# Optimization experiments

Hardware: AMD Instinct MI355X
Metric: run time of the kernel (lower is better)

Reference implementation:

```python
import jax, jax.numpy as jnp
import numpy as np

B = 8       # complexes in batch
C = 32      # CDR residues per antibody
G = 2048    # antigen nodes per complex
D = 128     # encoded_dims
N_AB = B * C
N_AG = B * G
N = N_AB + N_AG
SLOPE = 0.2
EPS_BN = 1e-5


def _build_edges():
    # block-sparse bipartite edges (cdr_b x ag_b), symmetrized, + self loops
    srcs, dsts = [], []
    for b in range(B):
        ab = np.arange(b * C, (b + 1) * C)
        ag = np.arange(N_AB + b * G, N_AB + (b + 1) * G)
        g1, g2 = np.meshgrid(ab, ag, indexing='ij')
        srcs.append(g1.ravel()); dsts.append(g2.ravel())
    s = np.concatenate(srcs); d = np.concatenate(dsts)
    loops = np.arange(N)
    src = np.concatenate([s, d, loops]).astype(np.int32)
    dst = np.concatenate([d, s, loops]).astype(np.int32)
    return src, dst


def setup_inputs() -> dict:
    key = jax.random.key(0)
    ks = jax.random.split(key, 16)
    sc = 1.0 / np.sqrt(D)
    edge_src, edge_dst = _build_edges()
    return {
        'selected_ab': jax.random.normal(ks[0], (N_AB, D), jnp.float32),
        'x_ag': jax.random.normal(ks[1], (N_AG, D), jnp.float32),
        'W1': jax.random.normal(ks[2], (D, D), jnp.float32) * sc,
        'a_src1': jax.random.normal(ks[3], (D,), jnp.float32) * sc,
        'a_dst1': jax.random.normal(ks[4], (D,), jnp.float32) * sc,
        'b1': jnp.zeros((D,), jnp.float32),
        'W2': jax.random.normal(ks[5], (D, D), jnp.float32) * sc,
        'a_src2': jax.random.normal(ks[6], (D,), jnp.float32) * sc,
        'a_dst2': jax.random.normal(ks[7], (D,), jnp.float32) * sc,
        'b2': jnp.zeros((D,), jnp.float32),
        'bn_ab_g': jnp.ones((2 * D,), jnp.float32),
        'bn_ab_b': jnp.zeros((2 * D,), jnp.float32),
        'bn_ag_g': jnp.ones((2 * D,), jnp.float32),
        'bn_ag_b': jnp.zeros((2 * D,), jnp.float32),
        'fc_w': jax.random.normal(ks[8], (2 * D, 1), jnp.float32) * sc,
        'fc_b': jnp.zeros((1,), jnp.float32),
        'agfc_w': jax.random.normal(ks[9], (2 * D, 1), jnp.float32) * sc,
        'agfc_b': jnp.zeros((1,), jnp.float32),
        'edge_src': jnp.asarray(edge_src),
        'edge_dst': jnp.asarray(edge_dst),
    }


def _gat(x, W, a_s, a_d, b, src, dst):
    # PyG GATConv, heads=1, eval mode (dropout off)
    h = x @ W                                  # [N, D]
    al_s = h @ a_s                             # [N]
    al_d = h @ a_d                             # [N]
    e = jax.nn.leaky_relu(al_s[src] + al_d[dst], SLOPE)   # [E]
    m = jax.ops.segment_max(e, dst, num_segments=N)
    e = jnp.exp(e - m[dst])
    z = jax.ops.segment_sum(e, dst, num_segments=N)
    alpha = e / (z[dst] + 1e-16)
    out = jax.ops.segment_sum(h[src] * alpha[:, None], dst, num_segments=N)
    return out + b


def _bn(x, g, b):
    # training-mode batch stats (biased variance), like torch BatchNorm1d
    m = x.mean(0)
    v = ((x - m) ** 2).mean(0)
    return (x - m) / jnp.sqrt(v + EPS_BN) * g + b


def reference(selected_ab, x_ag, W1, a_src1, a_dst1, b1, W2, a_src2, a_dst2, b2,
              bn_ab_g, bn_ab_b, bn_ag_g, bn_ag_b, fc_w, fc_b, agfc_w, agfc_b,
              edge_src, edge_dst):
    x = jnp.concatenate([selected_ab, x_ag], axis=0)          # [N, D]
    x = jax.nn.relu(_gat(x, W1, a_src1, a_dst1, b1, edge_src, edge_dst))
    x = _gat(x, W2, a_src2, a_dst2, b2, edge_src, edge_dst)
    x_ab = jnp.concatenate([x[:N_AB], selected_ab], axis=1)   # [N_ab, 2D]
    x_ab = jax.nn.relu(_bn(x_ab, bn_ab_g, bn_ab_b))
    x_ab = (x_ab @ fc_w + fc_b).ravel()
    x_ag_o = jnp.concatenate([x[N_AB:], x_ag], axis=1)        # [N_ag, 2D]
    x_ag_o = jax.nn.relu(_bn(x_ag_o, bn_ag_g, bn_ag_b))
    x_ag_o = (x_ag_o @ agfc_w + agfc_b).ravel()
    return (x_ab, x_ag_o)
```

## Files before the change

kernel.cpp:

```cpp
#include <hip/hip_runtime.h>


#define N_AB 256
#define N_AG 16384
#define N_ALL 16640
#define G_AG 2048
#define SLOPE 0.2f
#define MSHIFT 20.0f
#define GRID_F 512

typedef __attribute__((ext_vector_type(4))) float f32x4;
typedef __attribute__((ext_vector_type(8))) __bf16 bf16x8;
typedef __attribute__((ext_vector_type(8))) unsigned short u16x8;
typedef unsigned short ushort_t;

__device__ __forceinline__ float bf2f(ushort_t u) {
  union { unsigned int i; float f; } v; v.i = ((unsigned int)u) << 16; return v.f;
}
__device__ __forceinline__ ushort_t f2bf(float f) {
  union { float fv; unsigned int i; } v; v.fv = f;
  unsigned int x = v.i;
  return (ushort_t)((x + 0x7fffu + ((x >> 16) & 1u)) >> 16);
}
__device__ __forceinline__ float lrelu(float x) { return x >= 0.f ? x : SLOPE * x; }
__device__ __forceinline__ float expw(float e) {
  return __expf(fminf(e, 60.f) - MSHIFT);
}
__device__ __forceinline__ float ldf(const void* p, size_t i, int f) {
  return f ? ((const float*)p)[i] : bf2f(((const ushort_t*)p)[i]);
}
__device__ __forceinline__ void ld8f(const void* p, size_t i, int f, float* o) {
  if (f) {
    const f32x4* q = (const f32x4*)((const float*)p + i);
    f32x4 a = q[0], b = q[1];
#pragma unroll
    for (int j = 0; j < 4; ++j) { o[j] = a[j]; o[j + 4] = b[j]; }
  } else {
    u16x8 v = *(const u16x8*)((const ushort_t*)p + i);
#pragma unroll
    for (int j = 0; j < 8; ++j) o[j] = bf2f(v[j]);
  }
}

__device__ __forceinline__ void gbar(unsigned* __restrict__ ctr, int t) {
  __syncthreads();
  if (t == 0) {
    __threadfence();
    atomicAdd(ctr, 1u);
    while (atomicAdd(ctr, 0u) < (unsigned)GRID_F) __builtin_amdgcn_s_sleep(2);
  }
  __syncthreads();
  __threadfence();
}

__global__ __launch_bounds__(64) void k_init(unsigned* __restrict__ ctr) {
  if (threadIdx.x < 16) ctr[threadIdx.x] = 0u;
}

#define ABP_STRIDE 72
#define AG_STRIDE 40
#define HS_OFF 5120
#define HS_STRIDE 136

__global__ __launch_bounds__(256, 2) void k_fused(
    const void* __restrict__ sel_ab, const void* __restrict__ x_ag,
    const void* __restrict__ W1, const void* __restrict__ as1,
    const void* __restrict__ ad1, const void* __restrict__ b1,
    const void* __restrict__ W2, const void* __restrict__ as2,
    const void* __restrict__ ad2, const void* __restrict__ b2,
    const void* __restrict__ gab, const void* __restrict__ bab,
    const void* __restrict__ gag, const void* __restrict__ bag,
    const void* __restrict__ fcw, const void* __restrict__ fcb,
    const void* __restrict__ agfcw, const void* __restrict__ agfcb,
    ushort_t* __restrict__ h, ushort_t* __restrict__ xb,
    ushort_t* __restrict__ W1t, ushort_t* __restrict__ W2t,
    float* __restrict__ va, float* __restrict__ als, float* __restrict__ ald,
    float* __restrict__ bnsumAG, float* __restrict__ statsAG,
    float* __restrict__ xabf, float* __restrict__ accf,
    float* __restrict__ accz,
    float* __restrict__ selpart, float* __restrict__ selpartq,
    float* __restrict__ abpart, float* __restrict__ abpartq,
    float* __restrict__ agpart, float* __restrict__ agpartq,
    unsigned* __restrict__ ctrs, void* __restrict__ out) {
  __shared__ ushort_t hT[13824];
  __shared__ float alsS[64];
  __shared__ float colsum[128], colsq[128];
  __shared__ float preLs[2][128], preLq[2][128];
  __shared__ float zsh[32], wsh[32];
  __shared__ float stA[256], stB[256], stW[256];

  int t = threadIdx.x, lane = t & 63, wid = t >> 6;
  int bx = blockIdx.x;
  int mm = lane & 15, q = lane >> 4;

  const ushort_t* selu = (const ushort_t*)sel_ab;
  int cnt = 0;
#pragma unroll
  for (int i = 0; i < 8; ++i) {
    unsigned e = (selu[lane * 8 + i] >> 7) & 0xFF;
    if (e > 0xC8) cnt++;
  }
  int f = (__popcll(__ballot(cnt > 0)) >= 3) ? 1 : 0;

  if (bx < 16) {
    const void* W = (bx < 8) ? W1 : W2;
    ushort_t* Wt = (bx < 8) ? W1t : W2t;
    int base = (bx & 7) * 2048 + t * 8;
    float o[8];
    ld8f(W, base, f, o);
#pragma unroll
    for (int j = 0; j < 8; ++j) {
      int idx = base + j;
      Wt[(idx & 127) * 128 + (idx >> 7)] = f2bf(o[j]);
    }
  } else if (bx < 32) {
    int j = bx - 16;
    const void* W   = (j < 8) ? W1 : W2;
    const void* asv = (j < 8) ? as1 : as2;
    const void* adv = (j < 8) ? ad1 : ad2;
    int vbase = (j < 8) ? 0 : 256;
    int basek = (j & 7) * 16 + wid * 4;
    float a_s0 = ldf(asv, lane, f), a_s1 = ldf(asv, lane + 64, f);
    float a_d0 = ldf(adv, lane, f), a_d1 = ldf(adv, lane + 64, f);
#pragma unroll
    for (int i = 0; i < 4; ++i) {
      int k = basek + i;
      float w0 = ldf(W, (size_t)k * 128 + lane, f);
      float w1 = ldf(W, (size_t)k * 128 + lane + 64, f);
      float ps = w0 * a_s0 + w1 * a_s1;
      float pd = w0 * a_d0 + w1 * a_d1;
#pragma unroll
      for (int o = 1; o < 64; o <<= 1) {
        ps += __shfl_xor(ps, o);
        pd += __shfl_xor(pd, o);
      }
      if (lane == 0) { va[vbase + k] = ps; va[vbase + 128 + k] = pd; }
    }
  } else if (bx < 40) {
    int j = bx - 32;
    f32x4* az = (f32x4*)(accf + (size_t)j * 4096);
    f32x4 z4 = (f32x4){0.f, 0.f, 0.f, 0.f};
    for (int i = t; i < 1024; i += 256) az[i] = z4;
    if (j == 0) { bnsumAG[t] = 0.f; bnsumAG[t + 256] = 0.f; accz[t] = 0.f; }
  } else if (bx < 48) {
    int j = bx - 40;
    int col = t & 127, rh = t >> 7;
    int r0 = j * 32 + rh * 16;
    float s = 0.f, sq = 0.f;
    for (int r = 0; r < 16; ++r) {
      float v = ldf(sel_ab, (size_t)(r0 + r) * 128 + col, f);
      s += v; sq += v * v;
    }
    preLs[rh][col] = s; preLq[rh][col] = sq;
    __syncthreads();
    if (t < 128) {
      selpart[j * 128 + t] = preLs[0][t] + preLs[1][t];
      selpartq[j * 128 + t] = preLq[0][t] + preLq[1][t];
    }
  } else if (bx < 112) {
    int j = bx - 48;
    int col = t & 127, half = t >> 7;
    int r0 = j * 256 + half * 128;
    float s = 0.f, sq = 0.f;
    for (int r = 0; r < 128; ++r) {
      float v = ldf(x_ag, (size_t)(r0 + r) * 128 + col, f);
      s += v; sq += v * v;
    }
    preLs[half][col] = s; preLq[half][col] = sq;
    __syncthreads();
    if (t < 128) {
      agpart[j * 128 + t] = preLs[0][t] + preLs[1][t];
      agpartq[j * 128 + t] = preLq[0][t] + preLq[1][t];
    }
  }
  gbar(&ctrs[0], t);

  auto gemm_tile = [&](int tile, const void* xa, int fxA, const void* xbv,
                       int fxB, const ushort_t* Wt, const float* vav) {
    int rw0 = tile * 32 + (wid >> 1) * 16;
    int ch = wid & 1;
    const void* xsrc; int roff, fx;
    if (rw0 < N_AB) { xsrc = xa; roff = rw0; fx = fxA; }
    else            { xsrc = xbv; roff = rw0 - N_AB; fx = fxB; }
    f32x4 acc[4];
#pragma unroll
    for (int b = 0; b < 4; ++b) acc[b] = (f32x4){0.f, 0.f, 0.f, 0.f};
    float pals = 0.f, pald = 0.f;
#pragma unroll
    for (int s = 0; s < 4; ++s) {
      int koff = s * 32 + q * 8;
      union { u16x8 u; bf16x8 b; } af;
      float o[8];
      ld8f(xsrc, (size_t)(roff + mm) * 128 + koff, fx, o);
#pragma unroll
      for (int j = 0; j < 8; ++j) {
        af.u[j] = f2bf(o[j]);
        pals += o[j] * vav[koff + j];
        pald += o[j] * vav[128 + koff + j];
      }
#pragma unroll
      for (int nt = 0; nt < 4; ++nt) {
        int colb = ch * 64 + nt * 16;
        bf16x8 bfr = *(const bf16x8*)(Wt + (size_t)(colb + mm) * 128 + koff);
        acc[nt] = __builtin_amdgcn_mfma_f32_16x16x32_bf16(af.b, bfr, acc[nt], 0, 0, 0);
      }
    }
    if (ch == 0) {
      float s1 = pals; s1 += __shfl_xor(s1, 16); s1 += __shfl_xor(s1, 32);
      float d1 = pald; d1 += __shfl_xor(d1, 16); d1 += __shfl_xor(d1, 32);
      if (lane < 16) { als[rw0 + lane] = s1; ald[rw0 + lane] = d1; }
    }
#pragma unroll
    for (int nt = 0; nt < 4; ++nt)
#pragma unroll
      for (int r = 0; r < 4; ++r) {
        int row = rw0 + q * 4 + r;
        int col = ch * 64 + nt * 16 + mm;
        h[(size_t)row * 128 + col] = f2bf(acc[nt][r]);
      }
  };

  auto agg_phase = [&](const void* bias, int do_relu, int do_bnsum) {
    if (bx < 256) {
      int b = bx >> 5, jt = bx & 31;
      int jbase = N_AB + b * G_AG + jt * 64;
      {
        int row = t & 31, c0g = (t >> 5) * 16;
        const ushort_t* src = h + (size_t)(b * 32 + row) * 128 + c0g;
        u16x8 v0 = *(const u16x8*)src;
        u16x8 v1 = *(const u16x8*)(src + 8);
#pragma unroll
        for (int j = 0; j < 8; ++j) {
          hT[(c0g + j) * AG_STRIDE + row] = v0[j];
          hT[(c0g + 8 + j) * AG_STRIDE + row] = v1[j];
        }
        ushort_t* hS = hT + HS_OFF;
        const ushort_t* hsrc = h + (size_t)jbase * 128;
#pragma unroll
        for (int it = 0; it < 4; ++it) {
          int e = it * 2048 + t * 8;
          int rr = e >> 7, cb = e & 127;
          *(u16x8*)&hS[rr * HS_STRIDE + cb] =
              *(const u16x8*)(hsrc + (size_t)rr * 128 + cb);
        }
        if (t < 32) alsS[t] = als[b * 32 + t];
        if (t < 128) { colsum[t] = 0.f; colsq[t] = 0.f; }
      }
      __syncthreads();
      int jl = jt * 64 + wid * 16;
      int jrow = N_AB + b * G_AG + jl;
      float aldj = ald[jrow + mm];
      float alsj = als[jrow + mm];
      union { u16x8 u; bf16x8 b; } af;
      float zp = 0.f;
#pragma unroll
      for (int j = 0; j < 8; ++j) {
        ushort_t us = f2bf(expw(lrelu(alsS[q * 8 + j] + aldj)));
        af.u[j] = us;
        zp += bf2f(us);
      }
      zp += __shfl_xor(zp, 16);
      zp += __shfl_xor(zp, 32);
      float wself = expw(lrelu(alsj + aldj));
      float z = zp + wself;
      float zin[4], wz[4];
#pragma unroll
      for (int r = 0; r < 4; ++r) {
        int rowl = q * 4 + r;
        float zr = __shfl(z, rowl);
        float wsr = __shfl(wself, rowl);
        float inv = 1.0f / (zr + 1e-16f);
        zin[r] = inv; wz[r] = wsr * inv;
      }
      const ushort_t* hSr = hT + HS_OFF + (size_t)(wid * 16) * HS_STRIDE;
#pragma unroll
      for (int nt = 0; nt < 8; ++nt) {
        int col = nt * 16 + mm;
        union { u16x8 u; bf16x8 b; } bfr;
        bfr.b = *(const bf16x8*)(&hT[col * AG_STRIDE + q * 8]);
        f32x4 acc = {0.f, 0.f, 0.f, 0.f};
        acc = __builtin_amdgcn_mfma_f32_16x16x32_bf16(af.b, bfr.b, acc, 0, 0, 0);
        float biasv = ldf(bias, col, f);
        float sl = 0.f, sq = 0.f;
#pragma unroll
        for (int r = 0; r < 4; ++r) {
          int row = q * 4 + r;
          float hv = bf2f(hSr[row * HS_STRIDE + col]);
          float v = acc[r] * zin[r] + wz[r] * hv + biasv;
          sl += v; sq += v * v;
          if (do_relu) v = fmaxf(v, 0.f);
          xb[(size_t)(jrow + row) * 128 + col] = f2bf(v);
        }
        if (do_bnsum) {
          atomicAdd(&colsum[col], sl);
          atomicAdd(&colsq[col], sq);
        }
      }
      if (do_bnsum) {
        __syncthreads();
        if (t < 128) {
          atomicAdd(&bnsumAG[t], colsum[t]);
          atomicAdd(&bnsumAG[256 + t], colsq[t]);
        }
      }
    } else {
      int bx2 = bx - 256;
      int b = bx2 >> 5, sg = bx2 & 31;
      int jrow0 = N_AB + b * G_AG + sg * 64;
      {
        int jr = t & 63, cgrp = (t >> 6) * 32;
        const ushort_t* src = h + (size_t)(jrow0 + jr) * 128 + cgrp;
#pragma unroll
        for (int v = 0; v < 4; ++v) {
          u16x8 vv = *(const u16x8*)(src + v * 8);
#pragma unroll
          for (int j = 0; j < 8; ++j)
            hT[(cgrp + v * 8 + j) * ABP_STRIDE + jr] = vv[j];
        }
        if (t < 64) alsS[t] = als[jrow0 + t];
      }
      __syncthreads();
      float aldm[2] = { ald[b * 32 + mm], ald[b * 32 + 16 + mm] };
      f32x4 acc[2][2];
#pragma unroll
      for (int a = 0; a < 2; ++a)
#pragma unroll
        for (int c = 0; c < 2; ++c) acc[a][c] = (f32x4){0.f, 0.f, 0.f, 0.f};
      float zz[2] = {0.f, 0.f};
#pragma unroll
      for (int s = 0; s < 2; ++s) {
        int k0 = s * 32 + q * 8;
        float a8[8];
#pragma unroll
        for (int j = 0; j < 8; ++j) a8[j] = alsS[k0 + j];
        union { u16x8 u; bf16x8 b; } af[2];
#pragma unroll
        for (int mt = 0; mt < 2; ++mt)
#pragma unroll
          for (int j = 0; j < 8; ++j) {
            ushort_t us = f2bf(expw(lrelu(a8[j] + aldm[mt])));
            af[mt].u[j] = us;
            zz[mt] += bf2f(us);
          }
#pragma unroll
        for (int ns = 0; ns < 2; ++ns) {
          int n = wid * 32 + ns * 16 + mm;
          union { u16x8 u; bf16x8 b; } bfr;
          bfr.b = *(const bf16x8*)(&hT[n * ABP_STRIDE + k0]);
          acc[0][ns] = __builtin_amdgcn_mfma_f32_16x16x32_bf16(af[0].b, bfr.b, acc[0][ns], 0, 0, 0);
          acc[1][ns] = __builtin_amdgcn_mfma_f32_16x16x32_bf16(af[1].b, bfr.b, acc[1][ns], 0, 0, 0);
        }
      }
#pragma unroll
      for (int mt = 0; mt < 2; ++mt)
#pragma unroll
        for (int ns = 0; ns < 2; ++ns)
#pragma unroll
          for (int r = 0; r < 4; ++r) {
            int row = b * 32 + mt * 16 + q * 4 + r;
            int col = wid * 32 + ns * 16 + mm;
            atomicAdd(&accf[(size_t)row * 128 + col], acc[mt][ns][r]);
          }
#pragma unroll
      for (int mt = 0; mt < 2; ++mt) {
        float z = zz[mt];
        z += __shfl_xor(z, 16);
        z += __shfl_xor(z, 32);
        if (wid == 0 && lane < 16)
          atomicAdd(&accz[b * 32 + mt * 16 + lane], z);
      }
    }
  };

  for (int tile = bx; tile < 520; tile += GRID_F)
    gemm_tile(tile, sel_ab, f, x_ag, f, W1t, va);
  gbar(&ctrs[1], t);

  agg_phase(b1, 1, 0);
  gbar(&ctrs[2], t);

  if (bx < 8) {
    int b = bx;
    if (t < 32) {
      int grow = b * 32 + t;
      float w = expw(lrelu(als[grow] + ald[grow]));
      zsh[t] = accz[grow] + w;
      wsh[t] = w;
      accz[grow] = 0.f;
    }
    __syncthreads();
#pragma unroll
    for (int i = 0; i < 16; ++i) {
      int e = i * 256 + t;
      int rl = e >> 7, col = e & 127;
      int grow = b * 32 + rl;
      size_t idx = (size_t)grow * 128 + col;
      float hv = bf2f(h[idx]);
      float v = (accf[idx] + wsh[rl] * hv) / (zsh[rl] + 1e-16f) + ldf(b1, col, f);
      accf[idx] = 0.f;
      v = fmaxf(v, 0.f);
      xabf[idx] = v;
    }
    __syncthreads();
  }
  for (int tile = bx; tile < 520; tile += GRID_F)
    gemm_tile(tile, xabf, 1, (const void*)(xb + (size_t)N_AB * 128), 0, W2t,
              va + 256);
  gbar(&ctrs[3], t);

  agg_phase(b2, 0, 1);
  gbar(&ctrs[4], t);

  if (bx < 33) {
    if (bx == 32) {
      float sB, sqB;
      if (t < 128) { sB = bnsumAG[t]; sqB = bnsumAG[256 + t]; }
      else {
        int c = t - 128;
        sB = 0.f; sqB = 0.f;
        for (int j = 0; j < 64; ++j) {
          sB += agpart[j * 128 + c];
          sqB += agpartq[j * 128 + c];
        }
      }
      float mean = sB * (1.f / 16384.f);
      float var = fmaxf(sqB * (1.f / 16384.f) - mean * mean, 0.f);
      float A = ldf(gag, t, f) / sqrtf(var + 1e-5f);
      statsAG[t] = A;
      statsAG[256 + t] = ldf(bag, t, f) - mean * A;
      statsAG[512 + t] = ldf(agfcw, t, f);
    } else {
      int b = bx >> 2, q4 = bx & 3;
      if (t < 8) {
        int grow = b * 32 + q4 * 8 + t;
        float w = expw(lrelu(als[grow] + ald[grow]));
        zsh[t] = accz[grow] + w;
        wsh[t] = w;
      }
      __syncthreads();
      float s = 0.f, sq = 0.f;
#pragma unroll
      for (int i = 0; i < 4; ++i) {
        int e = i * 256 + t;
        int rl = e >> 7, col = e & 127;
        int grow = b * 32 + q4 * 8 + rl;
        size_t idx = (size_t)grow * 128 + col;
        float hv = bf2f(h[idx]);
        float v = (accf[idx] + wsh[rl] * hv) / (zsh[rl] + 1e-16f) + ldf(b2, col, f);
        xabf[idx] = v;
        s += v; sq += v * v;
      }
      preLs[t >> 7][t & 127] = s;
      preLq[t >> 7][t & 127] = sq;
      __syncthreads();
      if (t < 128) {
        abpart[bx * 128 + t] = preLs[0][t] + preLs[1][t];
        abpartq[bx * 128 + t] = preLq[0][t] + preLq[1][t];
      }
    }
  }
  gbar(&ctrs[5], t);

  for (int g = bx; g < 1040; g += GRID_F) {
    __syncthreads();
    int isAb = (g < 16);
    if (isAb) {
      float s = 0.f, sq = 0.f;
      if (t < 128) {
        for (int j = 0; j < 32; ++j) {
          s += abpart[j * 128 + t];
          sq += abpartq[j * 128 + t];
        }
      } else {
        int c = t - 128;
        for (int j = 0; j < 8; ++j) {
          s += selpart[j * 128 + c];
          sq += selpartq[j * 128 + c];
        }
      }
      float mean = s * (1.f / 256.f);
      float var = fmaxf(sq * (1.f / 256.f) - mean * mean, 0.f);
      float A = ldf(gab, t, f) / sqrtf(var + 1e-5f);
      stA[t] = A;
      stB[t] = ldf(bab, t, f) - mean * A;
      stW[t] = ldf(fcw, t, f);
    } else {
      stA[t] = statsAG[t];
      stB[t] = statsAG[256 + t];
      stW[t] = statsAG[512 + t];
    }
    __syncthreads();
    int c0 = lane * 2;
    float a0 = stA[c0],        a1 = stA[c0 + 1];
    float a2 = stA[128 + c0],  a3 = stA[128 + c0 + 1];
    float g0 = stB[c0],        g1 = stB[c0 + 1];
    float g2 = stB[128 + c0],  g3 = stB[128 + c0 + 1];
    float w0 = stW[c0],        w1 = stW[c0 + 1];
    float w2 = stW[128 + c0],  w3 = stW[128 + c0 + 1];
    int row0 = isAb ? (g * 16 + wid * 4) : (N_AB + (g - 16) * 16 + wid * 4);
    float bb = isAb ? ldf(fcb, 0, f) : ldf(agfcb, 0, f);
#pragma unroll
    for (int i = 0; i < 4; ++i) {
      int row = row0 + i;
      float v0, v1, v2, v3;
      if (isAb) {
        const float* p = xabf + (size_t)row * 128 + c0;
        v0 = p[0]; v1 = p[1];
        size_t ro = (size_t)row * 128 + c0;
        v2 = ldf(sel_ab, ro, f);
        v3 = ldf(sel_ab, ro + 1, f);
      } else {
        const ushort_t* p = xb + (size_t)row * 128 + c0;
        v0 = bf2f(p[0]); v1 = bf2f(p[1]);
        size_t ro = (size_t)(row - N_AB) * 128 + c0;
        v2 = ldf(x_ag, ro, f);
        v3 = ldf(x_ag, ro + 1, f);
      }
      float acc =
          fmaxf(v0 * a0 + g0, 0.f) * w0
        + fmaxf(v1 * a1 + g1, 0.f) * w1
        + fmaxf(v2 * a2 + g2, 0.f) * w2
        + fmaxf(v3 * a3 + g3, 0.f) * w3;
#pragma unroll
      for (int o = 1; o < 64; o <<= 1) acc += __shfl_xor(acc, o);
      if (lane == 0) {
        float r = acc + bb;
        if (f) ((float*)out)[row] = r;
        else   ((ushort_t*)out)[row] = f2bf(r);
      }
    }
  }
}

__global__ __launch_bounds__(256) void k_pre(
    const void* __restrict__ W1, const void* __restrict__ W2,
    const void* __restrict__ as1, const void* __restrict__ ad1,
    const void* __restrict__ as2, const void* __restrict__ ad2,
    const void* __restrict__ sel_ab,
    ushort_t* __restrict__ W1t, ushort_t* __restrict__ W2t,
    float* __restrict__ va, float* __restrict__ bnsumAG,
    float* __restrict__ accf, float* __restrict__ accz,
    float* __restrict__ selpart, float* __restrict__ selpartq,
    int* __restrict__ flagp) {
  __shared__ float ls[2][128], lq[2][128];
  int t = threadIdx.x, lane = t & 63, wid = t >> 6;
  int bx = blockIdx.x;
  const ushort_t* selu = (const ushort_t*)sel_ab;
  int cnt = 0;
#pragma unroll
  for (int i = 0; i < 8; ++i) {
    unsigned e = (selu[lane * 8 + i] >> 7) & 0xFF;
    if (e > 0xC8) cnt++;
  }
  int f = (__popcll(__ballot(cnt > 0)) >= 3) ? 1 : 0;
  if (bx == 0 && t == 0) flagp[0] = f;

  if (bx < 16) {
    const void* W = (bx < 8) ? W1 : W2;
    ushort_t* Wt = (bx < 8) ? W1t : W2t;
    int base = (bx & 7) * 2048 + t * 8;
    float o[8];
    ld8f(W, base, f, o);
#pragma unroll
    for (int j = 0; j < 8; ++j) {
      int idx = base + j;
      Wt[(idx & 127) * 128 + (idx >> 7)] = f2bf(o[j]);
    }
  } else if (bx < 32) {
    int j = bx - 16;
    const void* W   = (j < 8) ? W1 : W2;
    const void* asv = (j < 8) ? as1 : as2;
    const void* adv = (j < 8) ? ad1 : ad2;
    int vbase = (j < 8) ? 0 : 256;
    int basek = (j & 7) * 16 + wid * 4;
    float a_s0 = ldf(asv, lane, f), a_s1 = ldf(asv, lane + 64, f);
    float a_d0 = ldf(adv, lane, f), a_d1 = ldf(adv, lane + 64, f);
#pragma unroll
    for (int i = 0; i < 4; ++i) {
      int k = basek + i;
      float w0 = ldf(W, (size_t)k * 128 + lane, f);
      float w1 = ldf(W, (size_t)k * 128 + lane + 64, f);
      float ps = w0 * a_s0 + w1 * a_s1;
      float pd = w0 * a_d0 + w1 * a_d1;
#pragma unroll
      for (int o = 1; o < 64; o <<= 1) {
        ps += __shfl_xor(ps, o);
        pd += __shfl_xor(pd, o);
      }
      if (lane == 0) { va[vbase + k] = ps; va[vbase + 128 + k] = pd; }
    }
  } else if (bx < 40) {
    int j = bx - 32;
    f32x4* az = (f32x4*)(accf + (size_t)j * 4096);
    f32x4 z4 = (f32x4){0.f, 0.f, 0.f, 0.f};
    for (int i = t; i < 1024; i += 256) az[i] = z4;
    if (j == 0) { bnsumAG[t] = 0.f; bnsumAG[t + 256] = 0.f; accz[t] = 0.f; }
  } else {
    int j = bx - 40;
    int col = t & 127, rh = t >> 7;
    int r0 = j * 32 + rh * 16;
    float s = 0.f, sq = 0.f;
    for (int r = 0; r < 16; ++r) {
      float v = ldf(sel_ab, (size_t)(r0 + r) * 128 + col, f);
      s += v; sq += v * v;
    }
    ls[rh][col] = s; lq[rh][col] = sq;
    __syncthreads();
    if (t < 128) {
      selpart[j * 128 + t] = ls[0][t] + ls[1][t];
      selpartq[j * 128 + t] = lq[0][t] + lq[1][t];
    }
  }
}

__global__ __launch_bounds__(256) void k_gemm(
    const void* __restrict__ xa, int modeA,
    const void* __restrict__ xb, int modeB,
    const int* __restrict__ flagp,
    const ushort_t* __restrict__ Wt, const float* __restrict__ va,
    ushort_t* __restrict__ h, float* __restrict__ als, float* __restrict__ ald,
    float* __restrict__ accf, float* __restrict__ accz,
    const void* __restrict__ biasAb, float* __restrict__ xabf, int do_abfin,
    const void* __restrict__ xraw, float* __restrict__ bnsumAG, int do_colsum) {
  __shared__ float zsh[32], wsh[32];
  int t = threadIdx.x, lane = t & 63, wid = t >> 6;
  int bx = blockIdx.x;

  if (do_colsum && bx < 64) {
    int fr = *flagp;
    int j = bx;
    int col = t & 127, half = t >> 7;
    int r0 = j * 256 + half * 128;
    float s = 0.f, sq = 0.f;
    for (int r = 0; r < 128; ++r) {
      float v = ldf(xraw, (size_t)(r0 + r) * 128 + col, fr);
      s += v; sq += v * v;
    }
    atomicAdd(&bnsumAG[128 + col], s);
    atomicAdd(&bnsumAG[384 + col], sq);
    return;
  }
  int gbx = do_colsum ? bx - 64 : bx;

  if (do_abfin && bx < 8) {
    int fr = *flagp;
    int b = bx;
    if (t < 32) {
      int grow = b * 32 + t;
      float w = expw(lrelu(als[grow] + ald[grow]));
      zsh[t] = accz[grow] + w;
      wsh[t] = w;
      accz[grow] = 0.f;
    }
    __syncthreads();
#pragma unroll
    for (int i = 0; i < 16; ++i) {
      int e = i * 256 + t;
      int rl = e >> 7, col = e & 127;
      int grow = b * 32 + rl;
      size_t idx = (size_t)grow * 128 + col;
      float hv = bf2f(h[idx]);
      float v = (accf[idx] + wsh[rl] * hv) / (zsh[rl] + 1e-16f) + ldf(biasAb, col, fr);
      accf[idx] = 0.f;
      v = fmaxf(v, 0.f);
      xabf[idx] = v;
    }
    __syncthreads();
  }

  int rw0 = gbx * 32 + (wid >> 1) * 16;
  int ch = wid & 1;
  const void* xsrc; int roff, mode;
  if (rw0 < N_AB) { xsrc = xa; roff = rw0; mode = modeA; }
  else            { xsrc = xb; roff = rw0 - N_AB; mode = modeB; }
  int fx = (mode == 2) ? *flagp : mode;
  int mm = lane & 15, q = lane >> 4;
  f32x4 acc[4];
#pragma unroll
  for (int b = 0; b < 4; ++b) acc[b] = (f32x4){0.f, 0.f, 0.f, 0.f};
  float pals = 0.f, pald = 0.f;
#pragma unroll
  for (int s = 0; s < 4; ++s) {
    int koff = s * 32 + q * 8;
    union { u16x8 u; bf16x8 b; } af;
    float o[8];
    ld8f(xsrc, (size_t)(roff + mm) * 128 + koff, fx, o);
#pragma unroll
    for (int j = 0; j < 8; ++j) {
      af.u[j] = f2bf(o[j]);
      pals += o[j] * va[koff + j];
      pald += o[j] * va[128 + koff + j];
    }
#pragma unroll
    for (int nt = 0; nt < 4; ++nt) {
      int colb = ch * 64 + nt * 16;
      bf16x8 bfr = *(const bf16x8*)(Wt + (size_t)(colb + mm) * 128 + koff);
      acc[nt] = __builtin_amdgcn_mfma_f32_16x16x32_bf16(af.b, bfr, acc[nt], 0, 0, 0);
    }
  }
  if (ch == 0) {
    float s1 = pals; s1 += __shfl_xor(s1, 16); s1 += __shfl_xor(s1, 32);
    float d1 = pald; d1 += __shfl_xor(d1, 16); d1 += __shfl_xor(d1, 32);
    if (lane < 16) { als[rw0 + lane] = s1; ald[rw0 + lane] = d1; }
  }
#pragma unroll
  for (int nt = 0; nt < 4; ++nt)
#pragma unroll
    for (int r = 0; r < 4; ++r) {
      int row = rw0 + q * 4 + r;
      int col = ch * 64 + nt * 16 + mm;
      h[(size_t)row * 128 + col] = f2bf(acc[nt][r]);
    }
}

__global__ __launch_bounds__(256) void k_agg(
    const ushort_t* __restrict__ h, const float* __restrict__ als,
    const float* __restrict__ ald, const void* __restrict__ bias,
    const int* __restrict__ flagp, ushort_t* __restrict__ xout,
    float* __restrict__ accf, float* __restrict__ accz,
    float* __restrict__ bnsumAG, int do_relu, int do_bnsum) {
  __shared__ ushort_t hT[13824];
  __shared__ float alsS[64];
  __shared__ float colsum[128], colsq[128];
  int bx = blockIdx.x;
  int t = threadIdx.x, lane = t & 63, wid = t >> 6;
  int mm = lane & 15, q = lane >> 4;

  if (bx < 256) {
    int b = bx >> 5, jt = bx & 31;
    int f = *flagp;
    int jbase = N_AB + b * G_AG + jt * 64;
    {
      int row = t & 31, c0g = (t >> 5) * 16;
      const ushort_t* src = h + (size_t)(b * 32 + row) * 128 + c0g;
      u16x8 v0 = *(const u16x8*)src;
      u16x8 v1 = *(const u16x8*)(src + 8);
#pragma unroll
      for (int j = 0; j < 8; ++j) {
        hT[(c0g + j) * AG_STRIDE + row] = v0[j];
        hT[(c0g + 8 + j) * AG_STRIDE + row] = v1[j];
      }
      ushort_t* hS = hT + HS_OFF;
      const ushort_t* hsrc = h + (size_t)jbase * 128;
#pragma unroll
      for (int it = 0; it < 4; ++it) {
        int e = it * 2048 + t * 8;
        int rr = e >> 7, cb = e & 127;
        *(u16x8*)&hS[rr * HS_STRIDE + cb] =
            *(const u16x8*)(hsrc + (size_t)rr * 128 + cb);
      }
      if (t < 32) alsS[t] = als[b * 32 + t];
      if (t < 128) { colsum[t] = 0.f; colsq[t] = 0.f; }
    }
    __syncthreads();
    int jl = jt * 64 + wid * 16;
    int jrow = N_AB + b * G_AG + jl;
    float aldj = ald[jrow + mm];
    float alsj = als[jrow + mm];
    union { u16x8 u; bf16x8 b; } af;
    float zp = 0.f;
#pragma unroll
    for (int j = 0; j < 8; ++j) {
      ushort_t us = f2bf(expw(lrelu(alsS[q * 8 + j] + aldj)));
      af.u[j] = us;
      zp += bf2f(us);
    }
    zp += __shfl_xor(zp, 16);
    zp += __shfl_xor(zp, 32);
    float wself = expw(lrelu(alsj + aldj));
    float z = zp + wself;
    float zin[4], wz[4];
#pragma unroll
    for (int r = 0; r < 4; ++r) {
      int rowl = q * 4 + r;
      float zr = __shfl(z, rowl);
      float wsr = __shfl(wself, rowl);
      float inv = 1.0f / (zr + 1e-16f);
      zin[r] = inv; wz[r] = wsr * inv;
    }
    const ushort_t* hSr = hT + HS_OFF + (size_t)(wid * 16) * HS_STRIDE;
#pragma unroll
    for (int nt = 0; nt < 8; ++nt) {
      int col = nt * 16 + mm;
      union { u16x8 u; bf16x8 b; } bfr;
      bfr.b = *(const bf16x8*)(&hT[col * AG_STRIDE + q * 8]);
      f32x4 acc = {0.f, 0.f, 0.f, 0.f};
      acc = __builtin_amdgcn_mfma_f32_16x16x32_bf16(af.b, bfr.b, acc, 0, 0, 0);
      float biasv = ldf(bias, col, f);
      float sl = 0.f, sq = 0.f;
#pragma unroll
      for (int r = 0; r < 4; ++r) {
        int row = q * 4 + r;
        float hv = bf2f(hSr[row * HS_STRIDE + col]);
        float v = acc[r] * zin[r] + wz[r] * hv + biasv;
        sl += v; sq += v * v;
        if (do_relu) v = fmaxf(v, 0.f);
        xout[(size_t)(jrow + row) * 128 + col] = f2bf(v);
      }
      if (do_bnsum) {
        atomicAdd(&colsum[col], sl);
        atomicAdd(&colsq[col], sq);
      }
    }
    if (do_bnsum) {
      __syncthreads();
      if (t < 128) {
        atomicAdd(&bnsumAG[t], colsum[t]);
        atomicAdd(&bnsumAG[256 + t], colsq[t]);
      }
    }
  } else {
    int bx2 = bx - 256;
    int b = bx2 >> 5, sg = bx2 & 31;
    int jrow0 = N_AB + b * G_AG + sg * 64;
    {
      int jr = t & 63, cgrp = (t >> 6) * 32;
      const ushort_t* src = h + (size_t)(jrow0 + jr) * 128 + cgrp;
#pragma unroll
      for (int v = 0; v < 4; ++v) {
        u16x8 vv = *(const u16x8*)(src + v * 8);
#pragma unroll
        for (int j = 0; j < 8; ++j)
          hT[(cgrp + v * 8 + j) * ABP_STRIDE + jr] = vv[j];
      }
      if (t < 64) alsS[t] = als[jrow0 + t];
    }
    __syncthreads();
    float aldm[2] = { ald[b * 32 + mm], ald[b * 32 + 16 + mm] };
    f32x4 acc[2][2];
#pragma unroll
    for (int a = 0; a < 2; ++a)
#pragma unroll
      for (int c = 0; c < 2; ++c) acc[a][c] = (f32x4){0.f, 0.f, 0.f, 0.f};
    float zz[2] = {0.f, 0.f};
#pragma unroll
    for (int s = 0; s < 2; ++s) {
      int k0 = s * 32 + q * 8;
      float a8[8];
#pragma unroll
      for (int j = 0; j < 8; ++j) a8[j] = alsS[k0 + j];
      union { u16x8 u; bf16x8 b; } af[2];
#pragma unroll
      for (int mt = 0; mt < 2; ++mt)
#pragma unroll
        for (int j = 0; j < 8; ++j) {
          ushort_t us = f2bf(expw(lrelu(a8[j] + aldm[mt])));
          af[mt].u[j] = us;
          zz[mt] += bf2f(us);
        }
#pragma unroll
      for (int ns = 0; ns < 2; ++ns) {
        int n = wid * 32 + ns * 16 + mm;
        union { u16x8 u; bf16x8 b; } bfr;
        bfr.b = *(const bf16x8*)(&hT[n * ABP_STRIDE + k0]);
        acc[0][ns] = __builtin_amdgcn_mfma_f32_16x16x32_bf16(af[0].b, bfr.b, acc[0][ns], 0, 0, 0);
        acc[1][ns] = __builtin_amdgcn_mfma_f32_16x16x32_bf16(af[1].b, bfr.b, acc[1][ns], 0, 0, 0);
      }
    }
#pragma unroll
    for (int mt = 0; mt < 2; ++mt)
#pragma unroll
      for (int ns = 0; ns < 2; ++ns)
#pragma unroll
        for (int r = 0; r < 4; ++r) {
          int row = b * 32 + mt * 16 + q * 4 + r;
          int col = wid * 32 + ns * 16 + mm;
          atomicAdd(&accf[(size_t)row * 128 + col], acc[mt][ns][r]);
        }
#pragma unroll
    for (int mt = 0; mt < 2; ++mt) {
      float z = zz[mt];
      z += __shfl_xor(z, 16);
      z += __shfl_xor(z, 32);
      if (wid == 0 && lane < 16)
        atomicAdd(&accz[b * 32 + mt * 16 + lane], z);
    }
  }
}

__global__ __launch_bounds__(256) void k_abfin(
    const float* __restrict__ accf, const float* __restrict__ accz,
    const ushort_t* __restrict__ h, const float* __restrict__ als,
    const float* __restrict__ ald, const void* __restrict__ bias,
    const int* __restrict__ flagp, float* __restrict__ xabf,
    float* __restrict__ abpart, float* __restrict__ abpartq,
    const float* __restrict__ bnsumAG,
    const void* __restrict__ gag, const void* __restrict__ bag,
    const void* __restrict__ agfcw, float* __restrict__ statsAG) {
  __shared__ float zsh[8], wsh[8];
  __shared__ float cs[2][128], cq[2][128];
  int bx = blockIdx.x, t = threadIdx.x;
  int f = *flagp;
  if (bx == 32) {
    float mean = bnsumAG[t] * (1.f / 16384.f);
    float var = fmaxf(bnsumAG[256 + t] * (1.f / 16384.f) - mean * mean, 0.f);
    float A = ldf(gag, t, f) / sqrtf(var + 1e-5f);
    statsAG[t] = A;
    statsAG[256 + t] = ldf(bag, t, f) - mean * A;
    statsAG[512 + t] = ldf(agfcw, t, f);
    return;
  }
  int b = bx >> 2, q4 = bx & 3;
  if (t < 8) {
    int grow = b * 32 + q4 * 8 + t;
    float w = expw(lrelu(als[grow] + ald[grow]));
    zsh[t] = accz[grow] + w;
    wsh[t] = w;
  }
  __syncthreads();
  float s = 0.f, sq = 0.f;
#pragma unroll
  for (int i = 0; i < 4; ++i) {
    int e = i * 256 + t;
    int rl = e >> 7, col = e & 127;
    int grow = b * 32 + q4 * 8 + rl;
    size_t idx = (size_t)grow * 128 + col;
    float hv = bf2f(h[idx]);
    float v = (accf[idx] + wsh[rl] * hv) / (zsh[rl] + 1e-16f) + ldf(bias, col, f);
    xabf[idx] = v;
    s += v; sq += v * v;
  }
  cs[t >> 7][t & 127] = s;
  cq[t >> 7][t & 127] = sq;
  __syncthreads();
  if (t < 128) {
    abpart[bx * 128 + t] = cs[0][t] + cs[1][t];
    abpartq[bx * 128 + t] = cq[0][t] + cq[1][t];
  }
}

__global__ __launch_bounds__(256) void k_head(
    const float* __restrict__ xfab, const ushort_t* __restrict__ xfag,
    const void* __restrict__ sel_ab, const void* __restrict__ x_ag,
    const float* __restrict__ statsAG,
    const float* __restrict__ selpart, const float* __restrict__ selpartq,
    const float* __restrict__ abpart, const float* __restrict__ abpartq,
    const void* __restrict__ gab, const void* __restrict__ bab,
    const void* __restrict__ fcw,
    const void* __restrict__ fcb, const void* __restrict__ agfcb,
    const int* __restrict__ flagp, void* __restrict__ out) {
  __shared__ float stA[256], stB[256], stW[256];
  int t = threadIdx.x, lane = t & 63, wid = t >> 6;
  int f = *flagp;
  int isAb = (blockIdx.x < 16);
  if (isAb) {
    float s = 0.f, sq = 0.f;
    if (t < 128) {
      for (int j = 0; j < 32; ++j) {
        s += abpart[j * 128 + t];
        sq += abpartq[j * 128 + t];
      }
    } else {
      int c = t - 128;
      for (int j = 0; j < 8; ++j) {
        s += selpart[j * 128 + c];
        sq += selpartq[j * 128 + c];
      }
    }
    float mean = s * (1.f / 256.f);
    float var = fmaxf(sq * (1.f / 256.f) - mean * mean, 0.f);
    float A = ldf(gab, t, f) / sqrtf(var + 1e-5f);
    stA[t] = A;
    stB[t] = ldf(bab, t, f) - mean * A;
    stW[t] = ldf(fcw, t, f);
  } else {
    stA[t] = statsAG[t];
    stB[t] = statsAG[256 + t];
    stW[t] = statsAG[512 + t];
  }
  __syncthreads();

  int c0 = lane * 2;
  float a0 = stA[c0],        a1 = stA[c0 + 1];
  float a2 = stA[128 + c0],  a3 = stA[128 + c0 + 1];
  float g0 = stB[c0],        g1 = stB[c0 + 1];
  float g2 = stB[128 + c0],  g3 = stB[128 + c0 + 1];
  float w0 = stW[c0],        w1 = stW[c0 + 1];
  float w2 = stW[128 + c0],  w3 = stW[128 + c0 + 1];
  int row0 = isAb ? (blockIdx.x * 16 + wid * 4)
                  : (N_AB + (blockIdx.x - 16) * 16 + wid * 4);
  float bb = isAb ? ldf(fcb, 0, f) : ldf(agfcb, 0, f);
#pragma unroll
  for (int i = 0; i < 4; ++i) {
    int row = row0 + i;
    float v0, v1, v2, v3;
    if (isAb) {
      const float* p = xfab + (size_t)row * 128 + c0;
      v0 = p[0]; v1 = p[1];
      size_t ro = (size_t)row * 128 + c0;
      v2 = ldf(sel_ab, ro, f);
      v3 = ldf(sel_ab, ro + 1, f);
    } else {
      const ushort_t* p = xfag + (size_t)row * 128 + c0;
      v0 = bf2f(p[0]); v1 = bf2f(p[1]);
      size_t ro = (size_t)(row - N_AB) * 128 + c0;
      v2 = ldf(x_ag, ro, f);
      v3 = ldf(x_ag, ro + 1, f);
    }
    float acc =
        fmaxf(v0 * a0 + g0, 0.f) * w0
      + fmaxf(v1 * a1 + g1, 0.f) * w1
      + fmaxf(v2 * a2 + g2, 0.f) * w2
      + fmaxf(v3 * a3 + g3, 0.f) * w3;
#pragma unroll
    for (int o = 1; o < 64; o <<= 1) acc += __shfl_xor(acc, o);
    if (lane == 0) {
      float r = acc + bb;
      if (f) ((float*)out)[row] = r;
      else   ((ushort_t*)out)[row] = f2bf(r);
    }
  }
}

extern "C" void kernel_launch(void* const* d_in, const int* in_sizes, int n_in,
                              void* d_out, int out_size, void* d_ws, size_t ws_size,
                              hipStream_t stream) {
  (void)in_sizes; (void)n_in; (void)out_size; (void)ws_size;
  const void* sel_ab = d_in[0];
  const void* x_ag   = d_in[1];
  const void* W1     = d_in[2];
  const void* as1    = d_in[3];
  const void* ad1    = d_in[4];
  const void* b1     = d_in[5];
  const void* W2     = d_in[6];
  const void* as2    = d_in[7];
  const void* ad2    = d_in[8];
  const void* b2     = d_in[9];
  const void* gab    = d_in[10];
  const void* bab    = d_in[11];
  const void* gag    = d_in[12];
  const void* bag    = d_in[13];
  const void* fcw    = d_in[14];
  const void* fcb    = d_in[15];
  const void* agfcw  = d_in[16];
  const void* agfcb  = d_in[17];

  ushort_t* h  = (ushort_t*)d_in[18];
  ushort_t* xb = (ushort_t*)d_in[19];

  char* wsp = (char*)d_ws;
  size_t off = 0;
  auto carve = [&](size_t bytes) -> char* {
    char* p = wsp + off; off += (bytes + 255) & ~(size_t)255; return p;
  };
  int* flag      = (int*)carve(64 * 4);
  ushort_t* W1t  = (ushort_t*)carve(16384 * 2);
  ushort_t* W2t  = (ushort_t*)carve(16384 * 2);
  float* va      = (float*)carve(512 * 4);
  float* als     = (float*)carve((size_t)N_ALL * 4);
  float* ald     = (float*)carve((size_t)N_ALL * 4);
  float* bnsumAG = (float*)carve(512 * 4);
  float* statsAG = (float*)carve(768 * 4);
  float* xabf    = (float*)carve((size_t)N_AB * 128 * 4);
  float* accf    = (float*)carve((size_t)N_AB * 128 * 4);
  float* accz    = (float*)carve(256 * 4);
  float* selpart = (float*)carve(8 * 128 * 4);
  float* selpartq= (float*)carve(8 * 128 * 4);
  float* abpart  = (float*)carve(32 * 128 * 4);
  float* abpartq = (float*)carve(32 * 128 * 4);
  float* agpart  = (float*)carve(64 * 128 * 4);
  float* agpartq = (float*)carve(64 * 128 * 4);
  unsigned* ctrs = (unsigned*)carve(16 * 4);

  static int fusedOK = -1;
  if (fusedOK < 0) {
    int nb = 0;
    hipError_t e = hipOccupancyMaxActiveBlocksPerMultiprocessor(&nb, k_fused, 256, 0);
    fusedOK = (e == hipSuccess && nb >= 2) ? 1 : 0;
  }

  if (fusedOK) {
    k_init<<<1, 64, 0, stream>>>(ctrs);
    k_fused<<<GRID_F, 256, 0, stream>>>(
        sel_ab, x_ag, W1, as1, ad1, b1, W2, as2, ad2, b2,
        gab, bab, gag, bag, fcw, fcb, agfcw, agfcb,
        h, xb, W1t, W2t, va, als, ald, bnsumAG, statsAG,
        xabf, accf, accz, selpart, selpartq, abpart, abpartq,
        agpart, agpartq, ctrs, d_out);
    return;
  }

  k_pre<<<48, 256, 0, stream>>>(W1, W2, as1, ad1, as2, ad2, sel_ab,
                                W1t, W2t, va, bnsumAG, accf, accz,
                                selpart, selpartq, flag);
  k_gemm<<<584, 256, 0, stream>>>(sel_ab, 2, x_ag, 2, flag, W1t, va, h, als, ald,
                                  accf, accz, b1, xabf, 0, x_ag, bnsumAG, 1);
  k_agg<<<512, 256, 0, stream>>>(h, als, ald, b1, flag, xb, accf, accz,
                                 bnsumAG, 1, 0);
  k_gemm<<<520, 256, 0, stream>>>(xabf, 1, xb + (size_t)N_AB * 128, 0, flag, W2t, va + 256, h, als, ald,
                                  accf, accz, b1, xabf, 1, x_ag, bnsumAG, 0);
  k_agg<<<512, 256, 0, stream>>>(h, als, ald, b2, flag, xb, accf, accz,
                                 bnsumAG, 0, 1);
  k_abfin<<<33, 256, 0, stream>>>(accf, accz, h, als, ald, b2, flag, xabf,
                                  abpart, abpartq, bnsumAG, gag, bag, agfcw,
                                  statsAG);
  k_head<<<1040, 256, 0, stream>>>(xabf, xb, sel_ab, x_ag, statsAG,
                                   selpart, selpartq, abpart, abpartq,
                                   gab, bab, fcw, fcb, agfcb, flag, d_out);
}
```

Measured before the change: 171.0 us.

## Use hierarchical grid barrier and size grid to one tile per block

Replaces the single-counter grid barrier with a two-level barrier: 8 leaf counters on separate cache lines, each taking 65 arrivals, and the last arrival on each leaf bumps a root counter that all blocks poll with relaxed loads. The grid grows from 512 to 520 blocks so each GEMM phase is exactly one tile per block, which removes the tail where 8 blocks did a second tile. Launch bounds are raised to 4 blocks per CU and the fused-path gate now requires at least 3. That stricter gate may push some configurations onto the slower multi-kernel fallback, and higher occupancy pressure may cause register spills.

```diff
diff --git a/kernel.cpp b/kernel.cpp
--- a/kernel.cpp
+++ b/kernel.cpp
@@ -7,7 +7,8 @@
 #define G_AG 2048
 #define SLOPE 0.2f
 #define MSHIFT 20.0f
-#define GRID_F 512
+#define GRID_F 520
+#define LEAF_N 65
 
 typedef __attribute__((ext_vector_type(4))) float f32x4;
 typedef __attribute__((ext_vector_type(8))) __bf16 bf16x8;
@@ -42,19 +43,21 @@
   }
 }
 
-__device__ __forceinline__ void gbar(unsigned* __restrict__ ctr, int t) {
+__device__ __forceinline__ void gbar(unsigned* __restrict__ base, int t, int bx) {
   __syncthreads();
   if (t == 0) {
     __threadfence();
-    atomicAdd(ctr, 1u);
-    while (atomicAdd(ctr, 0u) < (unsigned)GRID_F) __builtin_amdgcn_s_sleep(2);
+    unsigned v = atomicAdd(base + 32 * (1 + (bx & 7)), 1u);
+    if (v == (unsigned)(LEAF_N - 1)) atomicAdd(base, 1u);
+    while (__hip_atomic_load(base, __ATOMIC_RELAXED, __HIP_MEMORY_SCOPE_AGENT) < 8u)
+      __builtin_amdgcn_s_sleep(1);
   }
   __syncthreads();
   __threadfence();
 }
 
-__global__ __launch_bounds__(64) void k_init(unsigned* __restrict__ ctr) {
-  if (threadIdx.x < 16) ctr[threadIdx.x] = 0u;
+__global__ __launch_bounds__(256) void k_init(unsigned* __restrict__ ctr) {
+  for (int i = threadIdx.x; i < 2048; i += 256) ctr[i] = 0u;
 }
 
 #define ABP_STRIDE 72
@@ -62,7 +65,7 @@
 #define HS_OFF 5120
 #define HS_STRIDE 136
 
-__global__ __launch_bounds__(256, 2) void k_fused(
+__global__ __launch_bounds__(256, 4) void k_fused(
     const void* __restrict__ sel_ab, const void* __restrict__ x_ag,
     const void* __restrict__ W1, const void* __restrict__ as1,
     const void* __restrict__ ad1, const void* __restrict__ b1,
@@ -173,7 +176,7 @@
       agpartq[j * 128 + t] = preLq[0][t] + preLq[1][t];
     }
   }
-  gbar(&ctrs[0], t);
+  gbar(ctrs + 0 * 288, t, bx);
 
   auto gemm_tile = [&](int tile, const void* xa, int fxA, const void* xbv,
                        int fxB, const ushort_t* Wt, const float* vav) {
@@ -372,12 +375,11 @@
     }
   };
 
-  for (int tile = bx; tile < 520; tile += GRID_F)
-    gemm_tile(tile, sel_ab, f, x_ag, f, W1t, va);
-  gbar(&ctrs[1], t);
-
-  agg_phase(b1, 1, 0);
-  gbar(&ctrs[2], t);
+  gemm_tile(bx, sel_ab, f, x_ag, f, W1t, va);
+  gbar(ctrs + 1 * 288, t, bx);
+
+  if (bx < 512) agg_phase(b1, 1, 0);
+  gbar(ctrs + 2 * 288, t, bx);
 
   if (bx < 8) {
     int b = bx;
@@ -403,13 +405,12 @@
     }
     __syncthreads();
   }
-  for (int tile = bx; tile < 520; tile += GRID_F)
-    gemm_tile(tile, xabf, 1, (const void*)(xb + (size_t)N_AB * 128), 0, W2t,
-              va + 256);
-  gbar(&ctrs[3], t);
-
-  agg_phase(b2, 0, 1);
-  gbar(&ctrs[4], t);
+  gemm_tile(bx, xabf, 1, (const void*)(xb + (size_t)N_AB * 128), 0, W2t,
+            va + 256);
+  gbar(ctrs + 3 * 288, t, bx);
+
+  if (bx < 512) agg_phase(b2, 0, 1);
+  gbar(ctrs + 4 * 288, t, bx);
 
   if (bx < 33) {
     if (bx == 32) {
@@ -459,7 +460,7 @@
       }
     }
   }
-  gbar(&ctrs[5], t);
+  gbar(ctrs + 5 * 288, t, bx);
 
   for (int g = bx; g < 1040; g += GRID_F) {
     __syncthreads();
@@ -1060,17 +1061,17 @@
   float* abpartq = (float*)carve(32 * 128 * 4);
   float* agpart  = (float*)carve(64 * 128 * 4);
   float* agpartq = (float*)carve(64 * 128 * 4);
-  unsigned* ctrs = (unsigned*)carve(16 * 4);
+  unsigned* ctrs = (unsigned*)carve(2048 * 4);
 
   static int fusedOK = -1;
   if (fusedOK < 0) {
     int nb = 0;
     hipError_t e = hipOccupancyMaxActiveBlocksPerMultiprocessor(&nb, k_fused, 256, 0);
-    fusedOK = (e == hipSuccess && nb >= 2) ? 1 : 0;
+    fusedOK = (e == hipSuccess && nb >= 3) ? 1 : 0;
   }
 
   if (fusedOK) {
-    k_init<<<1, 64, 0, stream>>>(ctrs);
+    k_init<<<1, 256, 0, stream>>>(ctrs);
     k_fused<<<GRID_F, 256, 0, stream>>>(
         sel_ab, x_ag, W1, as1, ad1, b1, W2, as2, ad2, b2,
         gab, bab, gag, bag, fcw, fcb, agfcw, agfcb,
```

Result: no change. 169.4 us (-0.9%).
